# Kernel optimization log

Measured on AMD Instinct MI355X. Metric: run time of the kernel, lower is better.

## Reference

```python
import jax, jax.numpy as jnp
import numpy as np

B, S, D = 2, 2048, 2048
H, KV, HD = 32, 8, 64  # num_heads, num_key_value_heads, head_dim
ROPE_BASE = 10000.0


def setup_inputs() -> dict:
    key = jax.random.key(0)
    k1, k2, k3 = jax.random.split(key, 3)
    x = jax.random.normal(k1, (B, S, D), dtype=jnp.float32)
    # torch Linear weights are [out_features, in_features]
    w_qkv = jax.random.normal(k2, (H * HD + 2 * KV * HD, D), dtype=jnp.float32) * (D ** -0.5)
    w_out = jax.random.normal(k3, (D, D), dtype=jnp.float32) * (D ** -0.5)
    # true RoPE tables: cos/sin are [S, HD] with the half-frequencies duplicated
    inv_freq = 1.0 / (ROPE_BASE ** (jnp.arange(0, HD, 2, dtype=jnp.float32) / HD))
    angles = jnp.arange(S, dtype=jnp.float32)[:, None] * inv_freq[None, :]  # [S, HD/2]
    emb = jnp.concatenate([angles, angles], axis=-1)  # [S, HD]
    return {"x": x, "cos": jnp.cos(emb), "sin": jnp.sin(emb), "w_qkv": w_qkv, "w_out": w_out}


def _apply_rope(t, cos, sin):
    # t: [B, h, S, HD]; cos/sin: [S, HD]
    half = t.shape[-1] // 2
    t1, t2 = t[..., :half], t[..., half:]
    rot = jnp.concatenate([-t2, t1], axis=-1)
    return t * cos[None, None, :, :] + rot * sin[None, None, :, :]


def reference(x, cos, sin, w_qkv, w_out):
    b, s, d = x.shape
    qkv = jnp.einsum('bsd,od->bso', x, w_qkv)  # merged QKV projection
    q, k, v = jnp.split(qkv, [H * HD, H * HD + KV * HD], axis=-1)
    q = q.reshape(b, s, H, HD).transpose(0, 2, 1, 3)   # [b,H,s,hd]
    k = k.reshape(b, s, KV, HD).transpose(0, 2, 1, 3)  # [b,KV,s,hd]
    v = v.reshape(b, s, KV, HD).transpose(0, 2, 1, 3)
    q = _apply_rope(q, cos, sin)
    k = _apply_rope(k, cos, sin)
    n_rep = H // KV
    k = jnp.repeat(k, n_rep, axis=1)  # repeat_kv -> [b,H,s,hd]
    v = jnp.repeat(v, n_rep, axis=1)
    scale = HD ** -0.5
    scores = jnp.einsum('bhqd,bhkd->bhqk', q, k) * scale
    causal = jnp.tril(jnp.ones((s, s), dtype=bool))
    scores = jnp.where(causal[None, None], scores, jnp.finfo(scores.dtype).min)
    attn = jax.nn.softmax(scores, axis=-1)
    out = jnp.einsum('bhqk,bhkd->bhqd', attn, v)
    out = out.transpose(0, 2, 1, 3).reshape(b, s, H * HD)
    return jnp.einsum('bso,do->bsd', out, w_out)
```

## Files before the change

kernel.cpp:

```cpp
#include <hip/hip_runtime.h>
#include <hip/hip_fp16.h>

#define B_ 2
#define S_ 2048
#define D_ 2048
#define H_ 32
#define KV_ 8
#define HD_ 64

typedef unsigned short bf16_t;
typedef __attribute__((ext_vector_type(8))) short short8;
typedef __attribute__((ext_vector_type(4))) float floatx4;
typedef __attribute__((ext_vector_type(2))) float float2v;

__device__ __forceinline__ bf16_t f2bf(float f) {
  union { float f; unsigned u; } c; c.f = f;
  unsigned u = c.u;
  u += 0x7fffu + ((u >> 16) & 1u);
  return (bf16_t)(u >> 16);
}

__device__ __forceinline__ unsigned pk_bf16(float a, float b) {
#if __has_builtin(__builtin_amdgcn_cvt_pk_bf16_f32)
  auto v = __builtin_amdgcn_cvt_pk_bf16_f32(a, b);
  unsigned u; __builtin_memcpy(&u, &v, 4); return u;
#else
  return (unsigned)f2bf(a) | ((unsigned)f2bf(b) << 16);
#endif
}

__device__ __forceinline__ float fexp2(float x) {
#if __has_builtin(__builtin_amdgcn_exp2f)
  return __builtin_amdgcn_exp2f(x);
#else
  return exp2f(x);
#endif
}

__device__ __forceinline__ void load_lds16(const void* g, void* l) {
  __builtin_amdgcn_global_load_lds(
      (const __attribute__((address_space(1))) void*)g,
      (__attribute__((address_space(3))) void*)l, 16, 0, 0);
}

__device__ __forceinline__ void cvt4(const float* __restrict__ in,
                                     bf16_t* __restrict__ out, int i) {
  float4 v = ((const float4*)in)[i];
  ushort4 o;
  o.x = f2bf(v.x); o.y = f2bf(v.y); o.z = f2bf(v.z); o.w = f2bf(v.w);
  ((ushort4*)out)[i] = o;
}

__global__ __launch_bounds__(256) void prep(
    const float* __restrict__ x, bf16_t* __restrict__ xb,
    const float* __restrict__ wqkv, bf16_t* __restrict__ wqkvb,
    const float* __restrict__ wout, bf16_t* __restrict__ woutb,
    const float* __restrict__ cs, const float* __restrict__ sn,
    unsigned* __restrict__ tab) {
  const int bid = blockIdx.x;
  if (bid < 8192) {
    cvt4(x, xb, bid * 256 + threadIdx.x);
  } else if (bid < 14336) {
    cvt4(wqkv, wqkvb, (bid - 8192) * 256 + threadIdx.x);
  } else if (bid < 18432) {
    cvt4(wout, woutb, (bid - 14336) * 256 + threadIdx.x);
  } else {
    const int i = (bid - 18432) * 256 + threadIdx.x;
    __half2 h = __floats2half2_rn(cs[i], sn[i]);
    unsigned u; __builtin_memcpy(&u, &h, 4);
    tab[i] = u;
  }
}

__global__ __launch_bounds__(256) void gemm_bt(
    const bf16_t* __restrict__ A, const bf16_t* __restrict__ Bm,
    float* __restrict__ C, int M, int N, int K) {
  __shared__ __attribute__((aligned(16))) bf16_t As[128 * 32];
  __shared__ __attribute__((aligned(16))) bf16_t Bs[128 * 32];
  const int tid = threadIdx.x;
  const int lane = tid & 63;
  const int wave = tid >> 6;
  const int bm = blockIdx.y * 128, bn = blockIdx.x * 128;
  const int wm = (wave >> 1) * 64, wn = (wave & 1) * 64;
  const int lr = lane & 15, quad = lane >> 4;

  floatx4 acc[4][4] = {};

  const int t0 = tid, t1 = tid + 256;
  const int r0 = t0 >> 2, c0 = (t0 & 3) * 8;
  const int r1 = t1 >> 2, c1 = (t1 & 3) * 8;

  const bf16_t* Ab = A + (size_t)bm * K;
  const bf16_t* Bb = Bm + (size_t)bn * K;

  for (int k0 = 0; k0 < K; k0 += 32) {
    __syncthreads();
    load_lds16(Ab + (size_t)r0 * K + k0 + c0, &As[t0 * 8]);
    load_lds16(Ab + (size_t)r1 * K + k0 + c1, &As[t1 * 8]);
    load_lds16(Bb + (size_t)r0 * K + k0 + c0, &Bs[t0 * 8]);
    load_lds16(Bb + (size_t)r1 * K + k0 + c1, &Bs[t1 * 8]);
    __syncthreads();

    short8 af[4], bfr[4];
#pragma unroll
    for (int i = 0; i < 4; i++) {
      af[i]  = *(const short8*)&As[(wm + i * 16 + lr) * 32 + quad * 8];
      bfr[i] = *(const short8*)&Bs[(wn + i * 16 + lr) * 32 + quad * 8];
    }
#pragma unroll
    for (int mi = 0; mi < 4; mi++)
#pragma unroll
      for (int ni = 0; ni < 4; ni++)
        acc[mi][ni] = __builtin_amdgcn_mfma_f32_16x16x32_bf16(af[mi], bfr[ni], acc[mi][ni], 0, 0, 0);
  }

#pragma unroll
  for (int mi = 0; mi < 4; mi++) {
    const int row = bm + wm + mi * 16 + quad * 4;
#pragma unroll
    for (int ni = 0; ni < 4; ni++) {
      const int col = bn + wn + ni * 16 + lr;
      float* cp = C + (size_t)row * N + col;
#pragma unroll
      for (int r = 0; r < 4; r++) cp[(size_t)r * N] = acc[mi][ni][r];
    }
  }
}

__global__ __launch_bounds__(256) void gemm_qkv(
    const bf16_t* __restrict__ A, const bf16_t* __restrict__ Bm,
    const unsigned* __restrict__ tab,
    bf16_t* __restrict__ q, bf16_t* __restrict__ k, bf16_t* __restrict__ vt) {
  const int K = 2048;
  __shared__ __attribute__((aligned(16))) bf16_t As[128 * 32];
  __shared__ __attribute__((aligned(16))) bf16_t Bs[128 * 32];
  __shared__ __attribute__((aligned(16))) bf16_t Ts[4][64 * 72];
  const int tid = threadIdx.x;
  const int lane = tid & 63;
  const int wave = tid >> 6;
  const int bm = blockIdx.y * 128, bn = blockIdx.x * 128;
  const int wm = (wave >> 1) * 64, wn = (wave & 1) * 64;
  const int lr = lane & 15, quad = lane >> 4;

  floatx4 acc[4][4] = {};

  const int t0 = tid, t1 = tid + 256;
  const int r0 = t0 >> 2, c0 = (t0 & 3) * 8;
  const int r1 = t1 >> 2, c1 = (t1 & 3) * 8;

  const bf16_t* Ab = A + (size_t)bm * K;
  const bf16_t* Bb = Bm + (size_t)bn * K;

  for (int k0 = 0; k0 < K; k0 += 32) {
    __syncthreads();
    load_lds16(Ab + (size_t)r0 * K + k0 + c0, &As[t0 * 8]);
    load_lds16(Ab + (size_t)r1 * K + k0 + c1, &As[t1 * 8]);
    load_lds16(Bb + (size_t)r0 * K + k0 + c0, &Bs[t0 * 8]);
    load_lds16(Bb + (size_t)r1 * K + k0 + c1, &Bs[t1 * 8]);
    __syncthreads();

    short8 af[4], bfr[4];
#pragma unroll
    for (int i = 0; i < 4; i++) {
      af[i]  = *(const short8*)&As[(wm + i * 16 + lr) * 32 + quad * 8];
      bfr[i] = *(const short8*)&Bs[(wn + i * 16 + lr) * 32 + quad * 8];
    }
#pragma unroll
    for (int mi = 0; mi < 4; mi++)
#pragma unroll
      for (int ni = 0; ni < 4; ni++)
        acc[mi][ni] = __builtin_amdgcn_mfma_f32_16x16x32_bf16(af[mi], bfr[ni], acc[mi][ni], 0, 0, 0);
  }

  const int f0 = bn + wn;
  const int srow0 = bm + wm;
  const int bb = srow0 >> 11, s0 = srow0 & 2047;

  if (f0 < 2560) {
    const bool isq = (f0 < 2048);
    const float scale = isq ? 0.18033688011f : 1.0f;
    bf16_t* dst = isq ? (q + (size_t)(bb * H_ + (f0 >> 6)) * S_ * HD_)
                      : (k + (size_t)(bb * KV_ + ((f0 - 2048) >> 6)) * S_ * HD_);
#pragma unroll
    for (int mi = 0; mi < 4; mi++) {
#pragma unroll
      for (int r = 0; r < 4; r++) {
        const int sr = s0 + mi * 16 + quad * 4 + r;
        const unsigned* tp = tab + (size_t)sr * HD_;
        bf16_t* drow = dst + (size_t)sr * HD_;
#pragma unroll
        for (int ni = 0; ni < 4; ni++) {
          const int d = ni * 16 + lr;
          const unsigned w = tp[d];
          __half2 h2; __builtin_memcpy(&h2, &w, 4);
          const float2 cf = __half22float2(h2);
          const float t = acc[mi][ni][r];
          const float oth = acc[mi][ni ^ 2][r];
          const float rot = (ni < 2) ? -oth : oth;
          drow[d] = f2bf((t * cf.x + rot * cf.y) * scale);
        }
      }
    }
  } else {
    const int hv = (f0 - 2560) >> 6;
    bf16_t* ts = Ts[wave];
#pragma unroll
    for (int ni = 0; ni < 4; ni++)
#pragma unroll
      for (int mi = 0; mi < 4; mi++) {
        uint2 pw;
        pw.x = pk_bf16(acc[mi][ni][0], acc[mi][ni][1]);
        pw.y = pk_bf16(acc[mi][ni][2], acc[mi][ni][3]);
        *(uint2*)&ts[(ni * 16 + lr) * 72 + mi * 16 + quad * 4] = pw;
      }
    bf16_t* vrow = vt + ((size_t)(bb * KV_ + hv) * HD_ + lane) * S_ + s0;
#pragma unroll
    for (int j = 0; j < 8; j++)
      *(short8*)(vrow + j * 8) = *(const short8*)&ts[lane * 72 + j * 8];
  }
}

__device__ __forceinline__ void stage64(const bf16_t* __restrict__ gbase, int rstride,
                                        bf16_t* lbuf, int wave, int lane) {
  const int sub = lane >> 3;
  const int sc  = lane & 7;
  const int gc  = sc ^ sub;
#pragma unroll
  for (int j = 0; j < 2; j++) {
    const int r = wave * 16 + j * 8 + sub;
    load_lds16(gbase + (size_t)r * rstride + gc * 8,
               lbuf + (wave * 128 + j * 64 + lane) * 8);
  }
}

__device__ __forceinline__ void attn_qblock(
    const bf16_t* __restrict__ Q, const bf16_t* __restrict__ kb,
    const bf16_t* __restrict__ vb, bf16_t* __restrict__ O,
    bf16_t* Ks, bf16_t* Vs, bf16_t* pl,
    int bh, int q0, int wave, int lr, int quad) {
  const int b = bh >> 5, h = bh & 31;
  const int lane = quad * 16 + lr;
  const int sw = lr & 7;
  const bf16_t* qp = Q + ((size_t)bh * S_ + q0) * HD_;
  const short8 qf0 = *(const short8*)(qp + lr * HD_ + quad * 8);
  const short8 qf1 = *(const short8*)(qp + lr * HD_ + 32 + quad * 8);

  floatx4 o[4] = {};
  float m = -1e30f, l = 0.f;
  const int qg = q0 + lr;
  const int nt = (q0 >> 6) + 1;

  stage64(kb, HD_, Ks, wave, lane);
  stage64(vb, S_, Vs, wave, lane);

  for (int kt = 0; kt < nt; kt++) {
    const int kk = kt * 64;
    bf16_t* Kc = Ks + (kt & 1) * 4096;
    bf16_t* Vc = Vs + (kt & 1) * 4096;
    __syncthreads();
    if (kt + 1 < nt) {
      stage64(kb + (size_t)(kk + 64) * HD_, HD_, Ks + ((kt + 1) & 1) * 4096, wave, lane);
      stage64(vb + (kk + 64), S_, Vs + ((kt + 1) & 1) * 4096, wave, lane);
    }

    floatx4 st[4] = {};
#pragma unroll
    for (int t = 0; t < 4; t++) {
      const int R = t * 16 + lr;
      const short8 kf0 = *(const short8*)&Kc[R * 64 + ((quad ^ sw) * 8)];
      const short8 kf1 = *(const short8*)&Kc[R * 64 + (((4 + quad) ^ sw) * 8)];
      st[t] = __builtin_amdgcn_mfma_f32_16x16x32_bf16(kf0, qf0, st[t], 0, 0, 0);
      st[t] = __builtin_amdgcn_mfma_f32_16x16x32_bf16(kf1, qf1, st[t], 0, 0, 0);
    }
    if (kt == nt - 1) {
#pragma unroll
      for (int t = 0; t < 4; t++)
#pragma unroll
        for (int r = 0; r < 4; r++) {
          const int kg = kk + t * 16 + quad * 4 + r;
          st[t][r] = (kg <= qg) ? st[t][r] : -1e30f;
        }
    }
    float2v mx2 = { -3e30f, -3e30f };
#pragma unroll
    for (int t = 0; t < 4; t++) {
      const float2v lo = { st[t][0], st[t][1] };
      const float2v hi = { st[t][2], st[t][3] };
      mx2 = __builtin_elementwise_max(mx2, __builtin_elementwise_max(lo, hi));
    }
    float mx = fmaxf(mx2.x, mx2.y);
    mx = fmaxf(mx, __shfl_xor(mx, 16, 64));
    mx = fmaxf(mx, __shfl_xor(mx, 32, 64));
    const float mn = fmaxf(m, mx);
    const float2v mn2 = { mn, mn };
    float2v rs2 = { 0.f, 0.f };
#pragma unroll
    for (int t = 0; t < 4; t++) {
      float2v lo = { st[t][0], st[t][1] };
      float2v hi = { st[t][2], st[t][3] };
      lo = lo - mn2; hi = hi - mn2;
      const float p0 = fexp2(lo.x), p1 = fexp2(lo.y);
      const float p2 = fexp2(hi.x), p3 = fexp2(hi.y);
      st[t][0] = p0; st[t][1] = p1; st[t][2] = p2; st[t][3] = p3;
      const float2v pa = { p0, p1 }, pb = { p2, p3 };
      rs2 = rs2 + pa + pb;
    }
    float rs = rs2.x + rs2.y;
    rs += __shfl_xor(rs, 16, 64);
    rs += __shfl_xor(rs, 32, 64);
    if (__all(mn == m)) {
      l += rs;
    } else {
      const float a = fexp2(m - mn);
      l = l * a + rs;
      m = mn;
      const floatx4 a4 = { a, a, a, a };
#pragma unroll
      for (int dt = 0; dt < 4; dt++) o[dt] *= a4;
    }
#pragma unroll
    for (int t = 0; t < 4; t++) {
      uint2 pw;
      pw.x = pk_bf16(st[t][0], st[t][1]);
      pw.y = pk_bf16(st[t][2], st[t][3]);
      *(uint2*)&pl[lr * 64 + (((2 * t + (quad >> 1)) ^ sw) * 8) + (quad & 1) * 4] = pw;
    }
    const short8 pf0 = *(const short8*)&pl[lr * 64 + ((quad ^ sw) * 8)];
    const short8 pf1 = *(const short8*)&pl[lr * 64 + (((4 + quad) ^ sw) * 8)];
#pragma unroll
    for (int dt = 0; dt < 4; dt++) {
      const int Rv = dt * 16 + lr;
      const short8 vf0 = *(const short8*)&Vc[Rv * 64 + ((quad ^ sw) * 8)];
      const short8 vf1 = *(const short8*)&Vc[Rv * 64 + (((4 + quad) ^ sw) * 8)];
      o[dt] = __builtin_amdgcn_mfma_f32_16x16x32_bf16(vf0, pf0, o[dt], 0, 0, 0);
      o[dt] = __builtin_amdgcn_mfma_f32_16x16x32_bf16(vf1, pf1, o[dt], 0, 0, 0);
    }
  }

  const float linv = 1.f / l;
  const floatx4 lv = { linv, linv, linv, linv };
  bf16_t* ob = O + ((size_t)b * S_ + q0 + lr) * (H_ * HD_) + h * HD_ + quad * 4;
#pragma unroll
  for (int dt = 0; dt < 4; dt++) {
    const floatx4 ov = o[dt] * lv;
    uint2 pw;
    pw.x = pk_bf16(ov[0], ov[1]);
    pw.y = pk_bf16(ov[2], ov[3]);
    *(uint2*)(ob + dt * 16) = pw;
  }
}

__global__ __launch_bounds__(256, 4) void flash_attn(
    const bf16_t* __restrict__ Q,
    const bf16_t* __restrict__ Kc,
    const bf16_t* __restrict__ Vt,
    bf16_t* __restrict__ O) {
  __shared__ __attribute__((aligned(16))) bf16_t Ks[2 * 4096];
  __shared__ __attribute__((aligned(16))) bf16_t Vs[2 * 4096];
  __shared__ __attribute__((aligned(16))) bf16_t Pl[4][1024];
  const int bh = blockIdx.y;
  const int b = bh >> 5, h = bh & 31;
  const int kvh = b * KV_ + (h >> 2);
  const int wave = threadIdx.x >> 6, lane = threadIdx.x & 63;
  const int lr = lane & 15, quad = lane >> 4;

  const bf16_t* kb = Kc + (size_t)kvh * S_ * HD_;
  const bf16_t* vb = Vt + (size_t)kvh * HD_ * S_;
  bf16_t* pl = Pl[wave];

  const int ta = blockIdx.x;
  const int tb = 31 - blockIdx.x;
  attn_qblock(Q, kb, vb, O, Ks, Vs, pl, bh, ta * 64 + wave * 16, wave, lr, quad);
  __syncthreads();
  attn_qblock(Q, kb, vb, O, Ks, Vs, pl, bh, tb * 64 + wave * 16, wave, lr, quad);
}

extern "C" void kernel_launch(void* const* d_in, const int* in_sizes, int n_in,
                              void* d_out, int out_size, void* d_ws, size_t ws_size,
                              hipStream_t stream) {
  const float* x    = (const float*)d_in[0];
  const float* cs   = (const float*)d_in[1];
  const float* sn   = (const float*)d_in[2];
  const float* wqkv = (const float*)d_in[3];
  const float* wout = (const float*)d_in[4];
  float* out = (float*)d_out;

  char* ws = (char*)d_ws;
  bf16_t*  xb    = (bf16_t*)(ws);
  bf16_t*  wqkvb = (bf16_t*)(ws + 16777216);
  bf16_t*  woutb = (bf16_t*)(ws + 29360128);
  bf16_t*  qb    = (bf16_t*)(ws + 37748736);
  bf16_t*  kb    = (bf16_t*)(ws + 54525952);
  bf16_t*  vtb   = (bf16_t*)(ws + 58720256);
  bf16_t*  attnb = (bf16_t*)(ws + 62914560);
  unsigned* tab  = (unsigned*)(ws + 79691776);

  prep<<<18944, 256, 0, stream>>>(x, xb, wqkv, wqkvb, wout, woutb, cs, sn, tab);
  gemm_qkv<<<dim3(24, 32), 256, 0, stream>>>(xb, wqkvb, tab, qb, kb, vtb);
  flash_attn<<<dim3(16, 64), 256, 0, stream>>>(qb, kb, vtb, attnb);
  gemm_bt<<<dim3(16, 32), 256, 0, stream>>>(attnb, woutb, out, 4096, 2048, 2048);
}
```

Baseline: 331.9 us.

## Process two query tiles per wave in flash attention to reuse K/V loads

Each wave now handles two 16-row query sub-tiles, 64 rows apart, within a 128-row block. Every K/V tile staged in LDS is reused for both score and PV MFMA chains, which halves LDS staging and barrier overhead per unit of work. The grid shrinks to 8x64 blocks and launch bounds drop to 2 waves per SIMD to make room for the extra registers. The QKV GEMM's V-transpose scratch is also halved by writing it in two passes, with occupancy hinted at 4. The cost is fewer blocks in flight and higher register pressure.

Result: faster. 309.5 us (-6.8%).

```diff
diff --git a/kernel.cpp b/kernel.cpp
--- a/kernel.cpp
+++ b/kernel.cpp
@@ -127,14 +127,14 @@
   }
 }
 
-__global__ __launch_bounds__(256) void gemm_qkv(
+__global__ __launch_bounds__(256, 4) void gemm_qkv(
     const bf16_t* __restrict__ A, const bf16_t* __restrict__ Bm,
     const unsigned* __restrict__ tab,
     bf16_t* __restrict__ q, bf16_t* __restrict__ k, bf16_t* __restrict__ vt) {
   const int K = 2048;
   __shared__ __attribute__((aligned(16))) bf16_t As[128 * 32];
   __shared__ __attribute__((aligned(16))) bf16_t Bs[128 * 32];
-  __shared__ __attribute__((aligned(16))) bf16_t Ts[4][64 * 72];
+  __shared__ __attribute__((aligned(16))) bf16_t Ts[4][32 * 72];
   const int tid = threadIdx.x;
   const int lane = tid & 63;
   const int wave = tid >> 6;
@@ -204,19 +204,25 @@
   } else {
     const int hv = (f0 - 2560) >> 6;
     bf16_t* ts = Ts[wave];
-#pragma unroll
-    for (int ni = 0; ni < 4; ni++)
-#pragma unroll
-      for (int mi = 0; mi < 4; mi++) {
-        uint2 pw;
-        pw.x = pk_bf16(acc[mi][ni][0], acc[mi][ni][1]);
-        pw.y = pk_bf16(acc[mi][ni][2], acc[mi][ni][3]);
-        *(uint2*)&ts[(ni * 16 + lr) * 72 + mi * 16 + quad * 4] = pw;
+    const int rl = lane >> 1, hf = lane & 1;
+#pragma unroll
+    for (int p = 0; p < 2; p++) {
+#pragma unroll
+      for (int nn = 0; nn < 2; nn++) {
+        const int ni = 2 * p + nn;
+#pragma unroll
+        for (int mi = 0; mi < 4; mi++) {
+          uint2 pw;
+          pw.x = pk_bf16(acc[mi][ni][0], acc[mi][ni][1]);
+          pw.y = pk_bf16(acc[mi][ni][2], acc[mi][ni][3]);
+          *(uint2*)&ts[(nn * 16 + lr) * 72 + mi * 16 + quad * 4] = pw;
+        }
       }
-    bf16_t* vrow = vt + ((size_t)(bb * KV_ + hv) * HD_ + lane) * S_ + s0;
-#pragma unroll
-    for (int j = 0; j < 8; j++)
-      *(short8*)(vrow + j * 8) = *(const short8*)&ts[lane * 72 + j * 8];
+      bf16_t* vrow = vt + ((size_t)(bb * KV_ + hv) * HD_ + p * 32 + rl) * S_ + s0 + hf * 32;
+#pragma unroll
+      for (int j = 0; j < 4; j++)
+        *(short8*)(vrow + j * 8) = *(const short8*)&ts[rl * 72 + hf * 32 + j * 8];
+    }
   }
 }
 
@@ -233,22 +239,92 @@
   }
 }
 
-__device__ __forceinline__ void attn_qblock(
+__device__ __forceinline__ void softmax_ps(
+    floatx4* st, bool diag, int qg, int kk, float& m, float& l,
+    floatx4* o, bf16_t* pl, int lr, int quad, int sw) {
+  if (diag) {
+#pragma unroll
+    for (int t = 0; t < 4; t++)
+#pragma unroll
+      for (int r = 0; r < 4; r++) {
+        const int kg = kk + t * 16 + quad * 4 + r;
+        st[t][r] = (kg <= qg) ? st[t][r] : -1e30f;
+      }
+  }
+  float mx = -3e30f;
+#pragma unroll
+  for (int t = 0; t < 4; t++)
+#pragma unroll
+    for (int r = 0; r < 4; r++) mx = fmaxf(mx, st[t][r]);
+  mx = fmaxf(mx, __shfl_xor(mx, 16, 64));
+  mx = fmaxf(mx, __shfl_xor(mx, 32, 64));
+  const float mn = fmaxf(m, mx);
+  float rs = 0.f;
+#pragma unroll
+  for (int t = 0; t < 4; t++)
+#pragma unroll
+    for (int r = 0; r < 4; r++) {
+      const float p = fexp2(st[t][r] - mn);
+      st[t][r] = p;
+      rs += p;
+    }
+  rs += __shfl_xor(rs, 16, 64);
+  rs += __shfl_xor(rs, 32, 64);
+  if (__all(mn == m)) {
+    l += rs;
+  } else {
+    const float a = fexp2(m - mn);
+    l = l * a + rs;
+    m = mn;
+    const floatx4 a4 = { a, a, a, a };
+#pragma unroll
+    for (int dt = 0; dt < 4; dt++) o[dt] *= a4;
+  }
+#pragma unroll
+  for (int t = 0; t < 4; t++) {
+    uint2 pw;
+    pw.x = pk_bf16(st[t][0], st[t][1]);
+    pw.y = pk_bf16(st[t][2], st[t][3]);
+    *(uint2*)&pl[lr * 64 + (((2 * t + (quad >> 1)) ^ sw) * 8) + (quad & 1) * 4] = pw;
+  }
+}
+
+__device__ __forceinline__ void store_o(
+    const floatx4* o, float l, bf16_t* __restrict__ O,
+    int b, int h, int q0, int lr, int quad) {
+  const float linv = 1.f / l;
+  const floatx4 lv = { linv, linv, linv, linv };
+  bf16_t* ob = O + ((size_t)b * S_ + q0 + lr) * (H_ * HD_) + h * HD_ + quad * 4;
+#pragma unroll
+  for (int dt = 0; dt < 4; dt++) {
+    const floatx4 ov = o[dt] * lv;
+    uint2 pw;
+    pw.x = pk_bf16(ov[0], ov[1]);
+    pw.y = pk_bf16(ov[2], ov[3]);
+    *(uint2*)(ob + dt * 16) = pw;
+  }
+}
+
+__device__ __forceinline__ void attn_half(
     const bf16_t* __restrict__ Q, const bf16_t* __restrict__ kb,
     const bf16_t* __restrict__ vb, bf16_t* __restrict__ O,
-    bf16_t* Ks, bf16_t* Vs, bf16_t* pl,
-    int bh, int q0, int wave, int lr, int quad) {
+    bf16_t* Ks, bf16_t* Vs, bf16_t* pla, bf16_t* plb,
+    int bh, int T, int wave, int lr, int quad) {
   const int b = bh >> 5, h = bh & 31;
   const int lane = quad * 16 + lr;
   const int sw = lr & 7;
-  const bf16_t* qp = Q + ((size_t)bh * S_ + q0) * HD_;
-  const short8 qf0 = *(const short8*)(qp + lr * HD_ + quad * 8);
-  const short8 qf1 = *(const short8*)(qp + lr * HD_ + 32 + quad * 8);
-
-  floatx4 o[4] = {};
-  float m = -1e30f, l = 0.f;
-  const int qg = q0 + lr;
-  const int nt = (q0 >> 6) + 1;
+  const int qa0 = T * 128 + wave * 16;
+  const int qb0 = qa0 + 64;
+  const bf16_t* qpa = Q + ((size_t)bh * S_ + qa0) * HD_;
+  const short8 qfa0 = *(const short8*)(qpa + lr * HD_ + quad * 8);
+  const short8 qfa1 = *(const short8*)(qpa + lr * HD_ + 32 + quad * 8);
+  const short8 qfb0 = *(const short8*)(qpa + (64 + lr) * HD_ + quad * 8);
+  const short8 qfb1 = *(const short8*)(qpa + (64 + lr) * HD_ + 32 + quad * 8);
+
+  floatx4 oa[4] = {}, ob[4] = {};
+  float ma = -1e30f, la = 0.f, mb = -1e30f, lb = 0.f;
+  const int qga = qa0 + lr, qgb = qb0 + lr;
+  const int nt = 2 * T + 2;
 
   stage64(kb, HD_, Ks, wave, lane);
   stage64(vb, S_, Vs, wave, lane);
@@ -262,102 +338,59 @@
       stage64(kb + (size_t)(kk + 64) * HD_, HD_, Ks + ((kt + 1) & 1) * 4096, wave, lane);
       stage64(vb + (kk + 64), S_, Vs + ((kt + 1) & 1) * 4096, wave, lane);
     }
-
-    floatx4 st[4] = {};
+    const bool doA  = (kt <= 2 * T);
+    const bool dgA  = (kt == 2 * T);
+    const bool dgB  = (kt == nt - 1);
+
+    floatx4 sta[4] = {}, stb[4] = {};
 #pragma unroll
     for (int t = 0; t < 4; t++) {
       const int R = t * 16 + lr;
       const short8 kf0 = *(const short8*)&Kc[R * 64 + ((quad ^ sw) * 8)];
       const short8 kf1 = *(const short8*)&Kc[R * 64 + (((4 + quad) ^ sw) * 8)];
-      st[t] = __builtin_amdgcn_mfma_f32_16x16x32_bf16(kf0, qf0, st[t], 0, 0, 0);
-      st[t] = __builtin_amdgcn_mfma_f32_16x16x32_bf16(kf1, qf1, st[t], 0, 0, 0);
-    }
-    if (kt == nt - 1) {
-#pragma unroll
-      for (int t = 0; t < 4; t++)
-#pragma unroll
-        for (int r = 0; r < 4; r++) {
-          const int kg = kk + t * 16 + quad * 4 + r;
-          st[t][r] = (kg <= qg) ? st[t][r] : -1e30f;
-        }
-    }
-    float2v mx2 = { -3e30f, -3e30f };
-#pragma unroll
-    for (int t = 0; t < 4; t++) {
-      const float2v lo = { st[t][0], st[t][1] };
-      const float2v hi = { st[t][2], st[t][3] };
-      mx2 = __builtin_elementwise_max(mx2, __builtin_elementwise_max(lo, hi));
-    }
-    float mx = fmaxf(mx2.x, mx2.y);
-    mx = fmaxf(mx, __shfl_xor(mx, 16, 64));
-    mx = fmaxf(mx, __shfl_xor(mx, 32, 64));
-    const float mn = fmaxf(m, mx);
-    const float2v mn2 = { mn, mn };
-    float2v rs2 = { 0.f, 0.f };
-#pragma unroll
-    for (int t = 0; t < 4; t++) {
-      float2v lo = { st[t][0], st[t][1] };
-      float2v hi = { st[t][2], st[t][3] };
-      lo = lo - mn2; hi = hi - mn2;
-      const float p0 = fexp2(lo.x), p1 = fexp2(lo.y);
-      const float p2 = fexp2(hi.x), p3 = fexp2(hi.y);
-      st[t][0] = p0; st[t][1] = p1; st[t][2] = p2; st[t][3] = p3;
-      const float2v pa = { p0, p1 }, pb = { p2, p3 };
-      rs2 = rs2 + pa + pb;
-    }
-    float rs = rs2.x + rs2.y;
-    rs += __shfl_xor(rs, 16, 64);
-    rs += __shfl_xor(rs, 32, 64);
-    if (__all(mn == m)) {
-      l += rs;
-    } else {
-      const float a = fexp2(m - mn);
-      l = l * a + rs;
-      m = mn;
-      const floatx4 a4 = { a, a, a, a };
-#pragma unroll
-      for (int dt = 0; dt < 4; dt++) o[dt] *= a4;
-    }
-#pragma unroll
-    for (int t = 0; t < 4; t++) {
-      uint2 pw;
-      pw.x = pk_bf16(st[t][0], st[t][1]);
-      pw.y = pk_bf16(st[t][2], st[t][3]);
-      *(uint2*)&pl[lr * 64 + (((2 * t + (quad >> 1)) ^ sw) * 8) + (quad & 1) * 4] = pw;
-    }
-    const short8 pf0 = *(const short8*)&pl[lr * 64 + ((quad ^ sw) * 8)];
-    const short8 pf1 = *(const short8*)&pl[lr * 64 + (((4 + quad) ^ sw) * 8)];
+      if (doA) {
+        sta[t] = __builtin_amdgcn_mfma_f32_16x16x32_bf16(kf0, qfa0, sta[t], 0, 0, 0);
+        sta[t] = __builtin_amdgcn_mfma_f32_16x16x32_bf16(kf1, qfa1, sta[t], 0, 0, 0);
+      }
+      stb[t] = __builtin_amdgcn_mfma_f32_16x16x32_bf16(kf0, qfb0, stb[t], 0, 0, 0);
+      stb[t] = __builtin_amdgcn_mfma_f32_16x16x32_bf16(kf1, qfb1, stb[t], 0, 0, 0);
+    }
+    if (doA) softmax_ps(sta, dgA, qga, kk, ma, la, oa, pla, lr, quad, sw);
+    softmax_ps(stb, dgB, qgb, kk, mb, lb, ob, plb, lr, quad, sw);
+
+    short8 pfa0, pfa1;
+    if (doA) {
+      pfa0 = *(const short8*)&pla[lr * 64 + ((quad ^ sw) * 8)];
+      pfa1 = *(const short8*)&pla[lr * 64 + (((4 + quad) ^ sw) * 8)];
+    }
+    const short8 pfb0 = *(const short8*)&plb[lr * 64 + ((quad ^ sw) * 8)];
+    const short8 pfb1 = *(const short8*)&plb[lr * 64 + (((4 + quad) ^ sw) * 8)];
 #pragma unroll
     for (int dt = 0; dt < 4; dt++) {
       const int Rv = dt * 16 + lr;
       const short8 vf0 = *(const short8*)&Vc[Rv * 64 + ((quad ^ sw) * 8)];
       const short8 vf1 = *(const short8*)&Vc[Rv * 64 + (((4 + quad) ^ sw) * 8)];
-      o[dt] = __builtin_amdgcn_mfma_f32_16x16x32_bf16(vf0, pf0, o[dt], 0, 0, 0);
-      o[dt] = __builtin_amdgcn_mfma_f32_16x16x32_bf16(vf1, pf1, o[dt], 0, 0, 0);
-    }
-  }
-
-  const float linv = 1.f / l;
-  const floatx4 lv = { linv, linv, linv, linv };
-  bf16_t* ob = O + ((size_t)b * S_ + q0 + lr) * (H_ * HD_) + h * HD_ + quad * 4;
-#pragma unroll
-  for (int dt = 0; dt < 4; dt++) {
-    const floatx4 ov = o[dt] * lv;
-    uint2 pw;
-    pw.x = pk_bf16(ov[0], ov[1]);
-    pw.y = pk_bf16(ov[2], ov[3]);
-    *(uint2*)(ob + dt * 16) = pw;
-  }
-}
-
-__global__ __launch_bounds__(256, 4) void flash_attn(
+      if (doA) {
+        oa[dt] = __builtin_amdgcn_mfma_f32_16x16x32_bf16(vf0, pfa0, oa[dt], 0, 0, 0);
+        oa[dt] = __builtin_amdgcn_mfma_f32_16x16x32_bf16(vf1, pfa1, oa[dt], 0, 0, 0);
+      }
+      ob[dt] = __builtin_amdgcn_mfma_f32_16x16x32_bf16(vf0, pfb0, ob[dt], 0, 0, 0);
+      ob[dt] = __builtin_amdgcn_mfma_f32_16x16x32_bf16(vf1, pfb1, ob[dt], 0, 0, 0);
+    }
+  }
+
+  store_o(oa, la, O, b, h, qa0, lr, quad);
+  store_o(ob, lb, O, b, h, qb0, lr, quad);
+}
+
+__global__ __launch_bounds__(256, 2) void flash_attn(
     const bf16_t* __restrict__ Q,
     const bf16_t* __restrict__ Kc,
     const bf16_t* __restrict__ Vt,
     bf16_t* __restrict__ O) {
   __shared__ __attribute__((aligned(16))) bf16_t Ks[2 * 4096];
   __shared__ __attribute__((aligned(16))) bf16_t Vs[2 * 4096];
-  __shared__ __attribute__((aligned(16))) bf16_t Pl[4][1024];
+  __shared__ __attribute__((aligned(16))) bf16_t Pl[8192];
   const int bh = blockIdx.y;
   const int b = bh >> 5, h = bh & 31;
   const int kvh = b * KV_ + (h >> 2);
@@ -366,13 +399,14 @@
 
   const bf16_t* kb = Kc + (size_t)kvh * S_ * HD_;
   const bf16_t* vb = Vt + (size_t)kvh * HD_ * S_;
-  bf16_t* pl = Pl[wave];
+  bf16_t* pla = Pl + wave * 2048;
+  bf16_t* plb = pla + 1024;
 
   const int ta = blockIdx.x;
-  const int tb = 31 - blockIdx.x;
-  attn_qblock(Q, kb, vb, O, Ks, Vs, pl, bh, ta * 64 + wave * 16, wave, lr, quad);
+  const int tb = 15 - blockIdx.x;
+  attn_half(Q, kb, vb, O, Ks, Vs, pla, plb, bh, ta, wave, lr, quad);
   __syncthreads();
-  attn_qblock(Q, kb, vb, O, Ks, Vs, pl, bh, tb * 64 + wave * 16, wave, lr, quad);
+  attn_half(Q, kb, vb, O, Ks, Vs, pla, plb, bh, tb, wave, lr, quad);
 }
 
 extern "C" void kernel_launch(void* const* d_in, const int* in_sizes, int n_in,
@@ -397,6 +431,6 @@
 
   prep<<<18944, 256, 0, stream>>>(x, xb, wqkv, wqkvb, wout, woutb, cs, sn, tab);
   gemm_qkv<<<dim3(24, 32), 256, 0, stream>>>(xb, wqkvb, tab, qb, kb, vtb);
-  flash_attn<<<dim3(16, 64), 256, 0, stream>>>(qb, kb, vtb, attnb);
+  flash_attn<<<dim3(8, 64), 256, 0, stream>>>(qb, kb, vtb, attnb);
   gemm_bt<<<dim3(16, 32), 256, 0, stream>>>(attnb, woutb, out, 4096, 2048, 2048);
 }
```
